# Optimization experiments

Hardware: AMD Instinct MI355X
Metric: run time of the kernel (lower is better)

The kernel has to match this reference:

```python
import jax, jax.numpy as jnp
import numpy as np
from jax import lax

B, D, T = 8, 128, 4096
Q, C = 30, 1024


def setup_inputs() -> dict:
    key = jax.random.key(0)
    k1, k2 = jax.random.split(key)
    x = jax.random.normal(k1, (B, D, T), dtype=jnp.float32)
    codebooks = jax.random.normal(k2, (Q, C, D), dtype=jnp.float32)
    return {"x": x, "codebooks": codebooks}


def _vq_step(residual, cb):
    # residual: [B, T, D], cb: [C, D]
    # argmin over squared euclidean distance; ||r||^2 term is constant per row
    scores = -2.0 * jnp.einsum("btd,cd->btc", residual, cb) + jnp.sum(cb * cb, axis=-1)  # [B,T,C]
    idx = jnp.argmin(scores, axis=-1)          # [B,T]
    quant = cb[idx]                            # [B,T,D] gather
    # commitment loss: mse(quantize.detach(), residual)
    loss = jnp.mean((lax.stop_gradient(quant) - residual) ** 2)
    # straight-through estimator
    quant_st = residual + lax.stop_gradient(quant - residual)
    new_residual = residual - lax.stop_gradient(quant)
    return new_residual, (quant_st, loss)


def reference(x, codebooks):
    # x: [B, D, T] -> [B, T, D]
    xt = jnp.transpose(x, (0, 2, 1))
    _, (quants, losses) = lax.scan(_vq_step, xt, codebooks)  # quants: [Q,B,T,D]
    quantized = jnp.sum(quants, axis=0)                      # [B,T,D]
    quantized = jnp.transpose(quantized, (0, 2, 1))          # [B,D,T]
    commit_loss = jnp.sum(losses)
    return quantized, commit_loss
```

## Files before the change

kernel.cpp:

```cpp
#include <hip/hip_runtime.h>
#include <stdint.h>

#define B_ 8
#define D_ 128
#define T_ 4096
#define Q_ 30
#define C_ 1024

typedef __attribute__((ext_vector_type(8))) _Float16 half8;
typedef __attribute__((ext_vector_type(4))) float float4_;

__device__ __align__(16) _Float16 g_half[(size_t)Q_*C_*D_];

__global__ void rvq_prep(const float* __restrict__ cb, float* __restrict__ sumsq){
  int g    = blockIdx.x*128 + (threadIdx.x>>1);
  int half = threadIdx.x & 1;
  const float* src = cb + (size_t)g*D_ + half*64;
  double s = 0.0;
#pragma unroll
  for (int i=0;i<64;i+=4){
    float4_ f = *(const float4_*)(src+i);
    s += (double)f.x*f.x + (double)f.y*f.y + (double)f.z*f.z + (double)f.w*f.w;
  }
  s += __shfl_xor(s, 1);
  if (!half) sumsq[g] = (float)s;
}

__global__ void rvq_h(const float* __restrict__ cb){
  const size_t i = ((size_t)blockIdx.x*256 + threadIdx.x)*8;
  float4_ f0 = *(const float4_*)(cb + i);
  float4_ f1 = *(const float4_*)(cb + i + 4);
  half8 h;
  h[0]=(_Float16)f0.x; h[1]=(_Float16)f0.y; h[2]=(_Float16)f0.z; h[3]=(_Float16)f0.w;
  h[4]=(_Float16)f1.x; h[5]=(_Float16)f1.y; h[6]=(_Float16)f1.z; h[7]=(_Float16)f1.w;
  *(half8*)(g_half + i) = h;
}

__global__ __launch_bounds__(256,1) void rvq_main(
    const float* __restrict__ x, const float* __restrict__ cb,
    const float* __restrict__ sumsq, double* __restrict__ lossAcc,
    float* __restrict__ out)
{
  __shared__ float sCS[4][32][34];
  __shared__ int   sI4[4][32][4];

  const int tid  = threadIdx.x;
  const int wv   = tid>>6;
  const int ln   = tid&63;
  const int col  = ln&15;
  const int quad = ln>>4;
  const int blk  = blockIdx.x;
  const int b    = blk>>5;
  const int t0   = ((blk&31)<<7) + (wv<<5);

  double rmast[2][4][8];
#pragma unroll
  for (int rt=0;rt<2;++rt){
    const int t = t0 + rt*16 + col;
#pragma unroll
    for (int kc=0;kc<4;++kc)
#pragma unroll
      for (int j=0;j<8;++j){
        const int d = kc*32 + quad*8 + j;
        rmast[rt][kc][j] = (double)x[((size_t)b*D_ + d)*T_ + t];
      }
  }

  half8 ah[2][4];
  auto makeAB = [&](){
#pragma unroll
    for (int rt=0;rt<2;++rt)
#pragma unroll
      for (int kc=0;kc<4;++kc){
        half8 h;
#pragma unroll
        for (int j=0;j<8;++j) h[j] = (_Float16)(float)rmast[rt][kc][j];
        ah[rt][kc] = h;
      }
  };
  makeAB();

  double lossd = 0.0;

  half8 bufA[8], bufB[8];
  float ccA[2],  ccB[2];

  const _Float16* cbh0 = g_half;
  const float*    ssq0 = sumsq;

  auto loadGroup = [&](const _Float16* cbh, const float* ssq, int g, half8* Bv, float* cc){
#pragma unroll
    for (int kc=0;kc<4;++kc)
#pragma unroll
      for (int ct=0;ct<2;++ct){
        const int n = g*32 + ct*16 + col;
        Bv[kc*2+ct] = *(const half8*)(cbh + n*128 + kc*32 + quad*8);
      }
#pragma unroll
    for (int ct=0;ct<2;++ct)
      cc[ct] = ssq[(g*2+ct)*16 + col];
  };

  loadGroup(cbh0, ssq0, 0, bufA, ccA);

  for (int q=0;q<Q_;++q){
    const float*    cbq = cb    + (size_t)q*C_*D_;
    const _Float16* cbh = g_half + (size_t)q*C_*D_;
    const float*    ssq = sumsq + q*C_;

    float p1[2][4], p2[2][4];
#pragma unroll
    for (int rt=0;rt<2;++rt)
#pragma unroll
      for (int rg=0;rg<4;++rg){ p1[rt][rg]=3.0e38f; p2[rt][rg]=3.0e38f; }

#pragma unroll
    for (int g=0; g<32; ++g){
      half8* cur = (g&1) ? bufB : bufA;
      float* ccc = (g&1) ? ccB  : ccA;
      if (g < 31){
        loadGroup(cbh, ssq, g+1, (g&1)?bufA:bufB, (g&1)?ccA:ccB);
      } else if (q+1 < Q_){
        loadGroup(cbh + C_*D_, ssq + C_, 0, (g&1)?bufA:bufB, (g&1)?ccA:ccB);
      }

      float4_ acc[2][2];
#pragma unroll
      for (int a=0;a<2;++a)
#pragma unroll
        for (int c2=0;c2<2;++c2) acc[a][c2] = (float4_){0.f,0.f,0.f,0.f};
#pragma unroll
      for (int kc=0;kc<4;++kc)
#pragma unroll
        for (int rt=0;rt<2;++rt)
#pragma unroll
          for (int ct=0;ct<2;++ct)
            acc[rt][ct] = __builtin_amdgcn_mfma_f32_16x16x32_f16(ah[rt][kc], cur[kc*2+ct], acc[rt][ct], 0,0,0);

#pragma unroll
      for (int ct=0;ct<2;++ct){
        const int cid = g*2 + ct;
#pragma unroll
        for (int rt=0;rt<2;++rt)
#pragma unroll
          for (int rg=0;rg<4;++rg){
            float sc = fmaf(-2.0f, acc[rt][ct][rg], ccc[ct]);
            unsigned u = (__builtin_bit_cast(unsigned, sc) & ~63u) | (unsigned)cid;
            float sp = __builtin_bit_cast(float, u);
            if (sp < p1[rt][rg]) { p2[rt][rg]=p1[rt][rg]; p1[rt][rg]=sp; }
            else if (sp < p2[rt][rg]) { p2[rt][rg]=sp; }
          }
      }
    }

#pragma unroll
    for (int rt=0;rt<2;++rt)
#pragma unroll
      for (int rg=0;rg<4;++rg){
        const int row = rt*16 + quad*4 + rg;
        sCS[wv][row][col*2+0] = p1[rt][rg];
        sCS[wv][row][col*2+1] = p2[rt][rg];
      }

    if (ln < 32){
      const int row = ln;
      float b0=3.0e38f,b1=3.0e38f,b2=3.0e38f,b3=3.0e38f;
      int   e0=0,e1=0,e2=0,e3=0;
#pragma unroll
      for (int c2=0;c2<32;++c2){
        const float sc = sCS[wv][row][c2];
        const int   id = (((__builtin_bit_cast(unsigned, sc)) & 63u)<<4) + (c2>>1);
        const bool l0 = (sc<b0);
        const bool l1 = (sc<b1);
        const bool l2 = (sc<b2);
        const bool l3 = (sc<b3);
        if (l3){
          b3 = l2 ? b2 : sc;  e3 = l2 ? e2 : id;
          if (l2){
            b2 = l1 ? b1 : sc;  e2 = l1 ? e1 : id;
            if (l1){
              b1 = l0 ? b0 : sc;  e1 = l0 ? e0 : id;
              if (l0){ b0 = sc; e0 = id; }
            }
          }
        }
      }
      sI4[wv][row][0]=e0; sI4[wv][row][1]=e1; sI4[wv][row][2]=e2; sI4[wv][row][3]=e3;
    }

#pragma unroll
    for (int rt=0;rt<2;++rt){
      const int m = rt*16 + col;
      double bestS = 1.0e300; int bestJ = 0x7fffffff;
#pragma unroll
      for (int cnd=0;cnd<4;++cnd){
        const int jj = sI4[wv][m][cnd];
        const float* p = cbq + ((size_t)jj<<7) + (quad<<3);
        double sd = 0.0;
#pragma unroll
        for (int kc=0;kc<4;++kc){
          float4_ a0 = *(const float4_*)(p + kc*32);
          float4_ a1 = *(const float4_*)(p + kc*32 + 4);
          float fv[8] = {a0.x,a0.y,a0.z,a0.w,a1.x,a1.y,a1.z,a1.w};
#pragma unroll
          for (int j=0;j<8;++j){
            double cd = (double)fv[j];
            sd += cd*(cd - 2.0*rmast[rt][kc][j]);
          }
        }
        sd += __shfl_xor(sd, 16); sd += __shfl_xor(sd, 32);
        if ((sd < bestS) || (sd == bestS && jj < bestJ)){ bestS = sd; bestJ = jj; }
      }
      const float* pw = cbq + ((size_t)bestJ<<7) + (quad<<3);
#pragma unroll
      for (int kc=0;kc<4;++kc){
        float4_ w0 = *(const float4_*)(pw + kc*32);
        float4_ w1 = *(const float4_*)(pw + kc*32 + 4);
        float fw[8] = {w0.x,w0.y,w0.z,w0.w,w1.x,w1.y,w1.z,w1.w};
#pragma unroll
        for (int j=0;j<8;++j){
          double rn = rmast[rt][kc][j] - (double)fw[j];
          rmast[rt][kc][j] = rn;
          lossd += rn*rn;
        }
      }
    }
    makeAB();
  }

#pragma unroll
  for (int rt=0;rt<2;++rt){
    const int t = t0 + rt*16 + col;
#pragma unroll
    for (int kc=0;kc<4;++kc)
#pragma unroll
      for (int j=0;j<8;++j){
        const int d = kc*32 + quad*8 + j;
        const size_t o = ((size_t)b*D_ + d)*T_ + t;
        out[o] = (float)((double)x[o] - rmast[rt][kc][j]);
      }
  }
#pragma unroll
  for (int mk=1; mk<64; mk<<=1) lossd += __shfl_xor(lossd, mk);
  if (ln==0) atomicAdd(lossAcc, lossd);
}

__global__ void rvq_fin(const double* __restrict__ lossAcc, float* __restrict__ out){
  out[(size_t)B_*D_*T_] = (float)(*lossAcc * (1.0/((double)B_*(double)D_*(double)T_)));
}

extern "C" void kernel_launch(void* const* d_in, const int* in_sizes, int n_in,
                              void* d_out, int out_size, void* d_ws, size_t ws_size,
                              hipStream_t stream) {
  const float* x  = (const float*)d_in[0];
  const float* cb = (const float*)d_in[1];
  float* out      = (float*)d_out;
  double* lossAcc = (double*)d_ws;
  float*  sumsq   = (float*)((char*)d_ws + 256);

  hipMemsetAsync(d_ws, 0, 256, stream);
  rvq_prep<<<Q_*C_/128, 256, 0, stream>>>(cb, sumsq);
  rvq_h   <<<(Q_*C_*D_)/(256*8), 256, 0, stream>>>(cb);
  rvq_main<<<(B_*T_)/128, 256, 0, stream>>>(x, cb, sumsq, lossAcc, out);
  rvq_fin <<<1, 1, 0, stream>>>(lossAcc, out);
}
```

Before: 1.562 ms.

## Halve rows per wave to double block count and occupancy in RVQ main kernel

Each wave now handles 16 time rows instead of 32, so the grid doubles from 256 to 512 blocks and launch bounds allow two blocks per CU. This targets underutilization: 256 blocks of one block each leave many of the MI355X's CUs idle or lightly loaded, and halving the double-precision residual registers makes room for more waves. In exchange, each B-fragment load of the codebook feeds only half as many MFMAs, so codebook traffic per unit of compute doubles and reuse drops.

```diff
diff --git a/kernel.cpp b/kernel.cpp
--- a/kernel.cpp
+++ b/kernel.cpp
@@ -36,13 +36,13 @@
   *(half8*)(g_half + i) = h;
 }
 
-__global__ __launch_bounds__(256,1) void rvq_main(
+__global__ __launch_bounds__(256,2) void rvq_main(
     const float* __restrict__ x, const float* __restrict__ cb,
     const float* __restrict__ sumsq, double* __restrict__ lossAcc,
     float* __restrict__ out)
 {
-  __shared__ float sCS[4][32][34];
-  __shared__ int   sI4[4][32][4];
+  __shared__ float sCS[4][16][34];
+  __shared__ int   sI4[4][16][4];
 
   const int tid  = threadIdx.x;
   const int wv   = tid>>6;
@@ -50,33 +50,28 @@
   const int col  = ln&15;
   const int quad = ln>>4;
   const int blk  = blockIdx.x;
-  const int b    = blk>>5;
-  const int t0   = ((blk&31)<<7) + (wv<<5);
-
-  double rmast[2][4][8];
-#pragma unroll
-  for (int rt=0;rt<2;++rt){
-    const int t = t0 + rt*16 + col;
-#pragma unroll
-    for (int kc=0;kc<4;++kc)
-#pragma unroll
-      for (int j=0;j<8;++j){
-        const int d = kc*32 + quad*8 + j;
-        rmast[rt][kc][j] = (double)x[((size_t)b*D_ + d)*T_ + t];
-      }
-  }
-
-  half8 ah[2][4];
+  const int b    = blk>>6;
+  const int t0   = ((blk&63)<<6) + (wv<<4);
+  const int t    = t0 + col;
+
+  double rmast[4][8];
+#pragma unroll
+  for (int kc=0;kc<4;++kc)
+#pragma unroll
+    for (int j=0;j<8;++j){
+      const int d = kc*32 + quad*8 + j;
+      rmast[kc][j] = (double)x[((size_t)b*D_ + d)*T_ + t];
+    }
+
+  half8 ah[4];
   auto makeAB = [&](){
 #pragma unroll
-    for (int rt=0;rt<2;++rt)
-#pragma unroll
-      for (int kc=0;kc<4;++kc){
-        half8 h;
-#pragma unroll
-        for (int j=0;j<8;++j) h[j] = (_Float16)(float)rmast[rt][kc][j];
-        ah[rt][kc] = h;
-      }
+    for (int kc=0;kc<4;++kc){
+      half8 h;
+#pragma unroll
+      for (int j=0;j<8;++j) h[j] = (_Float16)(float)rmast[kc][j];
+      ah[kc] = h;
+    }
   };
   makeAB();
 
@@ -84,9 +79,6 @@
 
   half8 bufA[8], bufB[8];
   float ccA[2],  ccB[2];
-
-  const _Float16* cbh0 = g_half;
-  const float*    ssq0 = sumsq;
 
   auto loadGroup = [&](const _Float16* cbh, const float* ssq, int g, half8* Bv, float* cc){
 #pragma unroll
@@ -101,18 +93,16 @@
       cc[ct] = ssq[(g*2+ct)*16 + col];
   };
 
-  loadGroup(cbh0, ssq0, 0, bufA, ccA);
+  loadGroup(g_half, sumsq, 0, bufA, ccA);
 
   for (int q=0;q<Q_;++q){
-    const float*    cbq = cb    + (size_t)q*C_*D_;
+    const float*    cbq = cb     + (size_t)q*C_*D_;
     const _Float16* cbh = g_half + (size_t)q*C_*D_;
-    const float*    ssq = sumsq + q*C_;
-
-    float p1[2][4], p2[2][4];
-#pragma unroll
-    for (int rt=0;rt<2;++rt)
-#pragma unroll
-      for (int rg=0;rg<4;++rg){ p1[rt][rg]=3.0e38f; p2[rt][rg]=3.0e38f; }
+    const float*    ssq = sumsq  + q*C_;
+
+    float p1[4], p2[4];
+#pragma unroll
+    for (int rg=0;rg<4;++rg){ p1[rg]=3.0e38f; p2[rg]=3.0e38f; }
 
 #pragma unroll
     for (int g=0; g<32; ++g){
@@ -124,45 +114,37 @@
         loadGroup(cbh + C_*D_, ssq + C_, 0, (g&1)?bufA:bufB, (g&1)?ccA:ccB);
       }
 
-      float4_ acc[2][2];
-#pragma unroll
-      for (int a=0;a<2;++a)
-#pragma unroll
-        for (int c2=0;c2<2;++c2) acc[a][c2] = (float4_){0.f,0.f,0.f,0.f};
+      float4_ acc[2];
+#pragma unroll
+      for (int ct=0;ct<2;++ct) acc[ct] = (float4_){0.f,0.f,0.f,0.f};
 #pragma unroll
       for (int kc=0;kc<4;++kc)
 #pragma unroll
-        for (int rt=0;rt<2;++rt)
-#pragma unroll
-          for (int ct=0;ct<2;++ct)
-            acc[rt][ct] = __builtin_amdgcn_mfma_f32_16x16x32_f16(ah[rt][kc], cur[kc*2+ct], acc[rt][ct], 0,0,0);
+        for (int ct=0;ct<2;++ct)
+          acc[ct] = __builtin_amdgcn_mfma_f32_16x16x32_f16(ah[kc], cur[kc*2+ct], acc[ct], 0,0,0);
 
 #pragma unroll
       for (int ct=0;ct<2;++ct){
         const int cid = g*2 + ct;
 #pragma unroll
-        for (int rt=0;rt<2;++rt)
-#pragma unroll
-          for (int rg=0;rg<4;++rg){
-            float sc = fmaf(-2.0f, acc[rt][ct][rg], ccc[ct]);
-            unsigned u = (__builtin_bit_cast(unsigned, sc) & ~63u) | (unsigned)cid;
-            float sp = __builtin_bit_cast(float, u);
-            if (sp < p1[rt][rg]) { p2[rt][rg]=p1[rt][rg]; p1[rt][rg]=sp; }
-            else if (sp < p2[rt][rg]) { p2[rt][rg]=sp; }
-          }
-      }
-    }
-
-#pragma unroll
-    for (int rt=0;rt<2;++rt)
-#pragma unroll
-      for (int rg=0;rg<4;++rg){
-        const int row = rt*16 + quad*4 + rg;
-        sCS[wv][row][col*2+0] = p1[rt][rg];
-        sCS[wv][row][col*2+1] = p2[rt][rg];
-      }
-
-    if (ln < 32){
+        for (int rg=0;rg<4;++rg){
+          float sc = fmaf(-2.0f, acc[ct][rg], ccc[ct]);
+          unsigned u = (__builtin_bit_cast(unsigned, sc) & ~63u) | (unsigned)cid;
+          float sp = __builtin_bit_cast(float, u);
+          if (sp < p1[rg]) { p2[rg]=p1[rg]; p1[rg]=sp; }
+          else if (sp < p2[rg]) { p2[rg]=sp; }
+        }
+      }
+    }
+
+#pragma unroll
+    for (int rg=0;rg<4;++rg){
+      const int row = quad*4 + rg;
+      sCS[wv][row][col*2+0] = p1[rg];
+      sCS[wv][row][col*2+1] = p2[rg];
+    }
+
+    if (ln < 16){
       const int row = ln;
       float b0=3.0e38f,b1=3.0e38f,b2=3.0e38f,b3=3.0e38f;
       int   e0=0,e1=0,e2=0,e3=0;
@@ -188,9 +170,8 @@
       sI4[wv][row][0]=e0; sI4[wv][row][1]=e1; sI4[wv][row][2]=e2; sI4[wv][row][3]=e3;
     }
 
-#pragma unroll
-    for (int rt=0;rt<2;++rt){
-      const int m = rt*16 + col;
+    {
+      const int m = col;
       double bestS = 1.0e300; int bestJ = 0x7fffffff;
 #pragma unroll
       for (int cnd=0;cnd<4;++cnd){
@@ -205,7 +186,7 @@
 #pragma unroll
           for (int j=0;j<8;++j){
             double cd = (double)fv[j];
-            sd += cd*(cd - 2.0*rmast[rt][kc][j]);
+            sd += cd*(cd - 2.0*rmast[kc][j]);
           }
         }
         sd += __shfl_xor(sd, 16); sd += __shfl_xor(sd, 32);
@@ -219,8 +200,8 @@
         float fw[8] = {w0.x,w0.y,w0.z,w0.w,w1.x,w1.y,w1.z,w1.w};
 #pragma unroll
         for (int j=0;j<8;++j){
-          double rn = rmast[rt][kc][j] - (double)fw[j];
-          rmast[rt][kc][j] = rn;
+          double rn = rmast[kc][j] - (double)fw[j];
+          rmast[kc][j] = rn;
           lossd += rn*rn;
         }
       }
@@ -229,17 +210,13 @@
   }
 
 #pragma unroll
-  for (int rt=0;rt<2;++rt){
-    const int t = t0 + rt*16 + col;
-#pragma unroll
-    for (int kc=0;kc<4;++kc)
-#pragma unroll
-      for (int j=0;j<8;++j){
-        const int d = kc*32 + quad*8 + j;
-        const size_t o = ((size_t)b*D_ + d)*T_ + t;
-        out[o] = (float)((double)x[o] - rmast[rt][kc][j]);
-      }
-  }
+  for (int kc=0;kc<4;++kc)
+#pragma unroll
+    for (int j=0;j<8;++j){
+      const int d = kc*32 + quad*8 + j;
+      const size_t o = ((size_t)b*D_ + d)*T_ + t;
+      out[o] = (float)((double)x[o] - rmast[kc][j]);
+    }
 #pragma unroll
   for (int mk=1; mk<64; mk<<=1) lossd += __shfl_xor(lossd, mk);
   if (ln==0) atomicAdd(lossAcc, lossd);
@@ -261,6 +238,6 @@
   hipMemsetAsync(d_ws, 0, 256, stream);
   rvq_prep<<<Q_*C_/128, 256, 0, stream>>>(cb, sumsq);
   rvq_h   <<<(Q_*C_*D_)/(256*8), 256, 0, stream>>>(cb);
-  rvq_main<<<(B_*T_)/128, 256, 0, stream>>>(x, cb, sumsq, lossAcc, out);
+  rvq_main<<<(B_*T_)/64, 256, 0, stream>>>(x, cb, sumsq, lossAcc, out);
   rvq_fin <<<1, 1, 0, stream>>>(lossAcc, out);
 }
```

New measurement: 2.309 ms. 47.8% more time.

## Encode full codeword index in score low bits, use branchless med3 top-k and batched rescoring

Applied to the files above, without the earlier changes.

Packs the full 10-bit codeword index into the low mantissa bits of each fp16-MFMA score, so the per-lane top-2 and the per-row top-4 merge become branchless fmed3/fmin chains with no separate index tracking. Shared-memory stores and loads become vectorized (float2/float4) with the row stride padded to 36. The fp64 rescoring of the four candidates now issues all gathers together and keeps four independent accumulators to expose memory and ALU parallelism. Dropping the min-blocks-per-CU hint from launch_bounds lets the compiler use more registers. Clearing 10 mantissa bits instead of 6 coarsens score precision, which could change which candidates survive, and the tie-breaking order among equal scores also changes.

```diff
diff --git a/kernel.cpp b/kernel.cpp
--- a/kernel.cpp
+++ b/kernel.cpp
@@ -9,6 +9,7 @@
 
 typedef __attribute__((ext_vector_type(8))) _Float16 half8;
 typedef __attribute__((ext_vector_type(4))) float float4_;
+typedef __attribute__((ext_vector_type(2))) float float2_;
 
 __device__ __align__(16) _Float16 g_half[(size_t)Q_*C_*D_];
 
@@ -36,12 +37,12 @@
   *(half8*)(g_half + i) = h;
 }
 
-__global__ __launch_bounds__(256,1) void rvq_main(
+__global__ __launch_bounds__(256) void rvq_main(
     const float* __restrict__ x, const float* __restrict__ cb,
     const float* __restrict__ sumsq, double* __restrict__ lossAcc,
     float* __restrict__ out)
 {
-  __shared__ float sCS[4][32][34];
+  __shared__ float sCS[4][32][36];
   __shared__ int   sI4[4][32][4];
 
   const int tid  = threadIdx.x;
@@ -139,16 +140,16 @@
 
 #pragma unroll
       for (int ct=0;ct<2;++ct){
-        const int cid = g*2 + ct;
+        const unsigned idc = ((unsigned)(g*2+ct))<<4;
 #pragma unroll
         for (int rt=0;rt<2;++rt)
 #pragma unroll
           for (int rg=0;rg<4;++rg){
             float sc = fmaf(-2.0f, acc[rt][ct][rg], ccc[ct]);
-            unsigned u = (__builtin_bit_cast(unsigned, sc) & ~63u) | (unsigned)cid;
+            unsigned u = (__builtin_bit_cast(unsigned, sc) & ~1023u) | idc | (unsigned)col;
             float sp = __builtin_bit_cast(float, u);
-            if (sp < p1[rt][rg]) { p2[rt][rg]=p1[rt][rg]; p1[rt][rg]=sp; }
-            else if (sp < p2[rt][rg]) { p2[rt][rg]=sp; }
+            p2[rt][rg] = __builtin_amdgcn_fmed3f(sp, p1[rt][rg], p2[rt][rg]);
+            p1[rt][rg] = fminf(sp, p1[rt][rg]);
           }
       }
     }
@@ -158,59 +159,75 @@
 #pragma unroll
       for (int rg=0;rg<4;++rg){
         const int row = rt*16 + quad*4 + rg;
-        sCS[wv][row][col*2+0] = p1[rt][rg];
-        sCS[wv][row][col*2+1] = p2[rt][rg];
+        *(float2_*)&sCS[wv][row][col*2] = (float2_){p1[rt][rg], p2[rt][rg]};
       }
 
     if (ln < 32){
       const int row = ln;
       float b0=3.0e38f,b1=3.0e38f,b2=3.0e38f,b3=3.0e38f;
-      int   e0=0,e1=0,e2=0,e3=0;
-#pragma unroll
-      for (int c2=0;c2<32;++c2){
-        const float sc = sCS[wv][row][c2];
-        const int   id = (((__builtin_bit_cast(unsigned, sc)) & 63u)<<4) + (c2>>1);
-        const bool l0 = (sc<b0);
-        const bool l1 = (sc<b1);
-        const bool l2 = (sc<b2);
-        const bool l3 = (sc<b3);
-        if (l3){
-          b3 = l2 ? b2 : sc;  e3 = l2 ? e2 : id;
-          if (l2){
-            b2 = l1 ? b1 : sc;  e2 = l1 ? e1 : id;
-            if (l1){
-              b1 = l0 ? b0 : sc;  e1 = l0 ? e0 : id;
-              if (l0){ b0 = sc; e0 = id; }
-            }
-          }
-        }
-      }
-      sI4[wv][row][0]=e0; sI4[wv][row][1]=e1; sI4[wv][row][2]=e2; sI4[wv][row][3]=e3;
+#pragma unroll
+      for (int i=0;i<8;++i){
+        float4_ v = *(const float4_*)&sCS[wv][row][i*4];
+#pragma unroll
+        for (int k2=0;k2<4;++k2){
+          const float sc = v[k2];
+          b3 = __builtin_amdgcn_fmed3f(sc, b2, b3);
+          b2 = __builtin_amdgcn_fmed3f(sc, b1, b2);
+          b1 = __builtin_amdgcn_fmed3f(sc, b0, b1);
+          b0 = fminf(sc, b0);
+        }
+      }
+      sI4[wv][row][0] = (int)(__builtin_bit_cast(unsigned, b0) & 1023u);
+      sI4[wv][row][1] = (int)(__builtin_bit_cast(unsigned, b1) & 1023u);
+      sI4[wv][row][2] = (int)(__builtin_bit_cast(unsigned, b2) & 1023u);
+      sI4[wv][row][3] = (int)(__builtin_bit_cast(unsigned, b3) & 1023u);
     }
 
 #pragma unroll
     for (int rt=0;rt<2;++rt){
       const int m = rt*16 + col;
-      double bestS = 1.0e300; int bestJ = 0x7fffffff;
-#pragma unroll
-      for (int cnd=0;cnd<4;++cnd){
-        const int jj = sI4[wv][m][cnd];
-        const float* p = cbq + ((size_t)jj<<7) + (quad<<3);
-        double sd = 0.0;
-#pragma unroll
-        for (int kc=0;kc<4;++kc){
-          float4_ a0 = *(const float4_*)(p + kc*32);
-          float4_ a1 = *(const float4_*)(p + kc*32 + 4);
-          float fv[8] = {a0.x,a0.y,a0.z,a0.w,a1.x,a1.y,a1.z,a1.w};
-#pragma unroll
-          for (int j=0;j<8;++j){
-            double cd = (double)fv[j];
-            sd += cd*(cd - 2.0*rmast[rt][kc][j]);
-          }
-        }
-        sd += __shfl_xor(sd, 16); sd += __shfl_xor(sd, 32);
-        if ((sd < bestS) || (sd == bestS && jj < bestJ)){ bestS = sd; bestJ = jj; }
-      }
+      const int jj0 = sI4[wv][m][0];
+      const int jj1 = sI4[wv][m][1];
+      const int jj2 = sI4[wv][m][2];
+      const int jj3 = sI4[wv][m][3];
+      double sd0=0.0, sd1=0.0, sd2=0.0, sd3=0.0;
+#pragma unroll
+      for (int kc=0;kc<4;++kc){
+        float fv0[8], fv1[8], fv2[8], fv3[8];
+        {
+          const float* q0 = cbq + ((size_t)jj0<<7) + (quad<<3) + kc*32;
+          const float* q1 = cbq + ((size_t)jj1<<7) + (quad<<3) + kc*32;
+          const float* q2 = cbq + ((size_t)jj2<<7) + (quad<<3) + kc*32;
+          const float* q3 = cbq + ((size_t)jj3<<7) + (quad<<3) + kc*32;
+          float4_ a0 = *(const float4_*)(q0), a1 = *(const float4_*)(q0+4);
+          float4_ b0v= *(const float4_*)(q1), b1v= *(const float4_*)(q1+4);
+          float4_ c0 = *(const float4_*)(q2), c1 = *(const float4_*)(q2+4);
+          float4_ d0 = *(const float4_*)(q3), d1 = *(const float4_*)(q3+4);
+          fv0[0]=a0.x;fv0[1]=a0.y;fv0[2]=a0.z;fv0[3]=a0.w;fv0[4]=a1.x;fv0[5]=a1.y;fv0[6]=a1.z;fv0[7]=a1.w;
+          fv1[0]=b0v.x;fv1[1]=b0v.y;fv1[2]=b0v.z;fv1[3]=b0v.w;fv1[4]=b1v.x;fv1[5]=b1v.y;fv1[6]=b1v.z;fv1[7]=b1v.w;
+          fv2[0]=c0.x;fv2[1]=c0.y;fv2[2]=c0.z;fv2[3]=c0.w;fv2[4]=c1.x;fv2[5]=c1.y;fv2[6]=c1.z;fv2[7]=c1.w;
+          fv3[0]=d0.x;fv3[1]=d0.y;fv3[2]=d0.z;fv3[3]=d0.w;fv3[4]=d1.x;fv3[5]=d1.y;fv3[6]=d1.z;fv3[7]=d1.w;
+        }
+#pragma unroll
+        for (int j=0;j<8;++j){
+          const double r2 = 2.0 * rmast[rt][kc][j];
+          double cd;
+          cd = (double)fv0[j]; sd0 += cd*(cd - r2);
+          cd = (double)fv1[j]; sd1 += cd*(cd - r2);
+          cd = (double)fv2[j]; sd2 += cd*(cd - r2);
+          cd = (double)fv3[j]; sd3 += cd*(cd - r2);
+        }
+      }
+      sd0 += __shfl_xor(sd0,16); sd0 += __shfl_xor(sd0,32);
+      sd1 += __shfl_xor(sd1,16); sd1 += __shfl_xor(sd1,32);
+      sd2 += __shfl_xor(sd2,16); sd2 += __shfl_xor(sd2,32);
+      sd3 += __shfl_xor(sd3,16); sd3 += __shfl_xor(sd3,32);
+
+      double bestS = sd0; int bestJ = jj0;
+      if ((sd1 < bestS) || (sd1 == bestS && jj1 < bestJ)){ bestS = sd1; bestJ = jj1; }
+      if ((sd2 < bestS) || (sd2 == bestS && jj2 < bestJ)){ bestS = sd2; bestJ = jj2; }
+      if ((sd3 < bestS) || (sd3 == bestS && jj3 < bestJ)){ bestS = sd3; bestJ = jj3; }
+
       const float* pw = cbq + ((size_t)bestJ<<7) + (quad<<3);
 #pragma unroll
       for (int kc=0;kc<4;++kc){
```

Result: slower. 2.401 ms (+53.7%).
